# Optimization experiments

Hardware: AMD Instinct MI355X
Metric: run time of the kernel (lower is better)

The kernel has to match this reference:

```python
import jax, jax.numpy as jnp
import numpy as np

B, N, FIN, FOUT = 64, 784, 64, 64
EPS = 1e-5
NEG = -1e9  # masked-logit fill (avoids -inf NaNs on isolated nodes)


def setup_inputs() -> dict:
    key = jax.random.key(0)
    ks = jax.random.split(key, 6)
    init = lambda k, shape, fan: (jax.random.normal(k, shape, jnp.float32) / np.float32(np.sqrt(fan)))
    return {
        "node_features": jax.random.normal(ks[0], (B, N, FIN), jnp.float32),
        "adjacency_matrix": jax.random.randint(ks[1], (N, N), 0, 2, jnp.int32),
        "W_self": init(ks[2], (FOUT, FIN), FIN),
        "b_self": jnp.zeros((FOUT,), jnp.float32),
        "W_nb": init(ks[3], (FOUT, FIN), FIN),
        "b_nb": jnp.zeros((FOUT,), jnp.float32),
        "a_src": init(ks[4], (FIN,), 2 * FIN),   # attention weight half acting on x_i
        "a_dst": init(ks[5], (FIN,), 2 * FIN),   # attention weight half acting on x_j
        "b_att": jnp.zeros((), jnp.float32),
        "ln_gamma": jnp.ones((FOUT,), jnp.float32),
        "ln_beta": jnp.zeros((FOUT,), jnp.float32),
    }


def reference(node_features, adjacency_matrix, W_self, b_self, W_nb, b_nb,
              a_src, a_dst, b_att, ln_gamma, ln_beta):
    # mask[i, j] = node j is a neighbor of node i
    mask = adjacency_matrix != 0  # [N, N]

    self_feats = node_features @ W_self.T + b_self      # [B, N, Fout]
    nb_proj = node_features @ W_nb.T + b_nb              # [B, N, Fout]

    # attention(cat[x_i, x_j]) == x_i @ a_src + x_j @ a_dst + b_att
    src = node_features @ a_src                          # [B, N]
    dst = node_features @ a_dst                          # [B, N]
    logits = src[:, :, None] + dst[:, None, :] + b_att   # [B, N, N]
    logits = jnp.where(mask[None], logits, NEG)
    # softmax over neighbors j; zero out non-edges (handles isolated nodes -> 0)
    w = jax.nn.softmax(logits, axis=2) * mask[None]
    agg = jnp.einsum('bij,bjf->bif', w, nb_proj)         # [B, N, Fout]

    combined = self_feats + agg                           # dropout: eval mode (identity)
    mu = combined.mean(-1, keepdims=True)
    var = combined.var(-1, keepdims=True)
    normed = (combined - mu) * jax.lax.rsqrt(var + EPS) * ln_gamma + ln_beta
    return jax.nn.relu(normed)
```

## Files before the change

### kernel.cpp

```cpp
#include <hip/hip_runtime.h>


typedef unsigned short u16;
typedef unsigned int u32;
typedef short bf16x8 __attribute__((ext_vector_type(8)));
typedef float f32x4 __attribute__((ext_vector_type(4)));

#define NNODE 784
#define MP 832
#define BUFU 13312

__device__ __forceinline__ float b2f(u16 h) {
  union { u32 u; float f; } v; v.u = ((u32)h) << 16; return v.f;
}
__device__ __forceinline__ u16 f2b(float f) {
  union { float f; u32 u; } v; v.f = f;
  u32 r = (v.u + 0x7FFFu + ((v.u >> 16) & 1u)) >> 16;
  return (u16)r;
}
__device__ __forceinline__ void gload16(const u16* g, u16* l) {
  __builtin_amdgcn_global_load_lds((const __attribute__((address_space(1))) u32*)g,
                                   (__attribute__((address_space(3))) u32*)l, 16, 0, 0);
}

__global__ __launch_bounds__(256) void k_pre(const int* __restrict__ adj,
                                             const float* __restrict__ Ws,
                                             const float* __restrict__ Wn,
                                             const float* __restrict__ X,
                                             const float* __restrict__ adst,
                                             u16* __restrict__ A,
                                             u16* __restrict__ W2,
                                             u16* __restrict__ Bt) {
  const int bid = blockIdx.x;
  const int t = threadIdx.x;
  if (bid < 364) {
    int idx8 = bid * 256 + t;
    int i = idx8 / 104, j8 = idx8 - i * 104;
    __align__(16) u16 o[8];
    if (i < NNODE && j8 < 98) {
      const int4* ap = (const int4*)(adj + (size_t)i * NNODE + j8 * 8);
      int4 a0 = ap[0], a1 = ap[1];
      o[0] = a0.x ? 0x3F80 : 0; o[1] = a0.y ? 0x3F80 : 0;
      o[2] = a0.z ? 0x3F80 : 0; o[3] = a0.w ? 0x3F80 : 0;
      o[4] = a1.x ? 0x3F80 : 0; o[5] = a1.y ? 0x3F80 : 0;
      o[6] = a1.z ? 0x3F80 : 0; o[7] = a1.w ? 0x3F80 : 0;
    } else {
#pragma unroll
      for (int q = 0; q < 8; ++q) o[q] = 0;
    }
    *(uint4*)(A + (size_t)i * MP + j8 * 8) = *(const uint4*)o;
    return;
  }
  if (bid == 364) {
    int f = t >> 2, cq = t & 3;
#pragma unroll
    for (int q = 0; q < 4; ++q) {
      int c = cq * 4 + q;
      int cs = c ^ (f & 7);
      const float* src = (cs < 8) ? (Ws + f * 64 + cs * 8) : (Wn + f * 64 + (cs - 8) * 8);
      float4 v0 = ((const float4*)src)[0], v1 = ((const float4*)src)[1];
      __align__(16) u16 ob[8];
      ob[0] = f2b(v0.x); ob[1] = f2b(v0.y); ob[2] = f2b(v0.z); ob[3] = f2b(v0.w);
      ob[4] = f2b(v1.x); ob[5] = f2b(v1.y); ob[6] = f2b(v1.z); ob[7] = f2b(v1.w);
      *(uint4*)(W2 + f * 128 + c * 8) = *(const uint4*)ob;
    }
    return;
  }
  __shared__ float Xs[64][68];
  __shared__ float ad[64];
  __shared__ float es[64];
  int bid2 = bid - 365;
  int b = bid2 / 13, jt = bid2 - b * 13;
  int j0 = jt * 64;
  if (b == 64) {
    int row = 4160 + (t >> 2), c = (t & 3) * 16;
    uint4 z; z.x = 0; z.y = 0; z.z = 0; z.w = 0;
    uint4* p = (uint4*)(Bt + (size_t)row * MP + j0 + c);
    p[0] = z; p[1] = z;
    return;
  }
  int jr = t >> 2, cg = t & 3;
  {
    int j = j0 + jr;
    float4 z4; z4.x = 0.f; z4.y = 0.f; z4.z = 0.f; z4.w = 0.f;
    float4 v0 = z4, v1 = z4, v2 = z4, v3 = z4;
    if (j < NNODE) {
      const float4* xp = (const float4*)(X + ((size_t)b * NNODE + j) * 64 + cg * 16);
      v0 = xp[0]; v1 = xp[1]; v2 = xp[2]; v3 = xp[3];
    }
    float4* d = (float4*)&Xs[jr][cg * 16];
    d[0] = v0; d[1] = v1; d[2] = v2; d[3] = v3;
  }
  if (t < 64) ad[t] = adst[t];
  __syncthreads();
  {
    float dot = 0.f;
#pragma unroll
    for (int q = 0; q < 16; ++q) dot += Xs[jr][cg * 16 + q] * ad[cg * 16 + q];
    dot += __shfl_xor(dot, 1);
    dot += __shfl_xor(dot, 2);
    if (cg == 0) es[jr] = (j0 + jr < NNODE) ? __expf(dot) : 0.f;
  }
  __syncthreads();
  {
    int f = t >> 2, jc = (t & 3) * 16;
    __align__(16) u16 ob[16];
#pragma unroll
    for (int q = 0; q < 16; ++q) ob[q] = f2b(es[jc + q] * Xs[jc + q][f]);
    u16* op = Bt + ((size_t)b * 64 + f) * MP + j0 + jc;
    *(uint4*)op = *(const uint4*)ob;
    *(uint4*)(op + 8) = *(const uint4*)(ob + 8);
  }
  if (t < 64) Bt[(size_t)(4096 + b) * MP + j0 + t] = f2b(es[t]);
}

__global__ __launch_bounds__(512, 6) void k_gt(const u16* __restrict__ A,
                                               const u16* __restrict__ Bt,
                                               const u16* __restrict__ W2g,
                                               const float* __restrict__ X,
                                               const float* __restrict__ bs,
                                               const float* __restrict__ bn,
                                               const float* __restrict__ gam,
                                               const float* __restrict__ bet,
                                               float* __restrict__ out) {
  __shared__ __align__(16) u16 lds[2 * BUFU];
  const int t = threadIdx.x;
  const int l = t & 63, w = t >> 6;
  const int g = l >> 4, l15 = l & 15;
  const int wr = w >> 2, wc = w & 3;

  int wg = (blockIdx.x & 7) * 52 + (blockIdx.x >> 3);
  const int bp = wg / 13;
  const int it = wg - bp * 13;
  const int i0 = it * 64;
  const int nb0 = bp * 128;
  const int nd0 = 4096 + 2 * bp;

  f32x4 acc[2][2];
#pragma unroll
  for (int mi = 0; mi < 2; ++mi)
#pragma unroll
    for (int ni = 0; ni < 2; ++ni) acc[mi][ni] = (f32x4){0.f, 0.f, 0.f, 0.f};
  f32x4 accD[2];
  accD[0] = (f32x4){0.f, 0.f, 0.f, 0.f};
  accD[1] = (f32x4){0.f, 0.f, 0.f, 0.f};

#define STAGE(kt_, buf_)                                                          \
  {                                                                               \
    int k0_ = (kt_) * 64;                                                         \
    u16* dA_ = lds + (buf_) * BUFU;                                               \
    u16* dB_ = dA_ + 4096;                                                        \
    { int r_ = t >> 3, c_ = t & 7;                                                \
      gload16(A + (size_t)(i0 + r_) * MP + k0_ + ((c_ ^ (r_ & 7)) * 8),           \
              dA_ + w * 512); }                                                   \
    _Pragma("unroll")                                                             \
    for (int h_ = 0; h_ < 2; ++h_) {                                              \
      int s_ = h_ * 512 + t; int r_ = s_ >> 3, c_ = s_ & 7;                       \
      gload16(Bt + (size_t)(nb0 + r_) * MP + k0_ + ((c_ ^ (r_ & 7)) * 8),         \
              dB_ + h_ * 4096 + w * 512); }                                       \
    if (w < 2) { int r_ = t >> 3, c_ = t & 7;                                     \
      gload16(Bt + (size_t)(nd0 + r_) * MP + k0_ + ((c_ ^ (r_ & 7)) * 8),         \
              dB_ + 8192 + w * 512); }                                            \
  }

  STAGE(0, 0);

  for (int kt = 0; kt < 13; ++kt) {
    int buf = kt & 1;
    if (kt < 12) {
      STAGE(kt + 1, buf ^ 1);
      if (w < 2) asm volatile("s_waitcnt vmcnt(4)" ::: "memory");
      else       asm volatile("s_waitcnt vmcnt(3)" ::: "memory");
    } else {
      asm volatile("s_waitcnt vmcnt(0)" ::: "memory");
    }
    __builtin_amdgcn_s_barrier();
    __builtin_amdgcn_sched_barrier(0);
    const u16* As = lds + buf * BUFU;
    const u16* Bs = As + 4096;
#pragma unroll
    for (int kk = 0; kk < 2; ++kk) {
      int q = kk * 4 + g;
      bf16x8 af[2], bfr[2];
#pragma unroll
      for (int mi = 0; mi < 2; ++mi) {
        int ra = wr * 32 + mi * 16 + l15;
        af[mi] = *(const bf16x8*)(As + ra * 64 + ((q ^ (ra & 7)) * 8));
      }
#pragma unroll
      for (int ni = 0; ni < 2; ++ni) {
        int rb = wc * 32 + ni * 16 + l15;
        bfr[ni] = *(const bf16x8*)(Bs + rb * 64 + ((q ^ (rb & 7)) * 8));
      }
#pragma unroll
      for (int mi = 0; mi < 2; ++mi)
#pragma unroll
        for (int ni = 0; ni < 2; ++ni)
          acc[mi][ni] = __builtin_amdgcn_mfma_f32_16x16x32_bf16(af[mi], bfr[ni], acc[mi][ni], 0, 0, 0);
      if (wc == 2 + kk) {
        int rd = 128 + l15;
        bf16x8 bd = *(const bf16x8*)(Bs + rd * 64 + ((q ^ (rd & 7)) * 8));
        accD[0] = __builtin_amdgcn_mfma_f32_16x16x32_bf16(af[0], bd, accD[0], 0, 0, 0);
        accD[1] = __builtin_amdgcn_mfma_f32_16x16x32_bf16(af[1], bd, accD[1], 0, 0, 0);
      }
    }
    __builtin_amdgcn_sched_barrier(0);
    __builtin_amdgcn_s_barrier();
  }
#undef STAGE

  u16* AB2 = lds;
  u16* W2l = lds + 16384;
  float (*denL)[2] = (float (*)[2])((char*)lds + 49152);

  if (wc == 2 && l15 < 2) {
#pragma unroll
    for (int mi = 0; mi < 2; ++mi)
#pragma unroll
      for (int j = 0; j < 4; ++j)
        denL[wr * 32 + mi * 16 + g * 4 + j][l15] = accD[mi][j];
  }
#pragma unroll
  for (int q2 = 0; q2 < 2; ++q2) {
    int s = q2 * 512 + t;
    int r = s >> 3, c = s & 7;
    int i = i0 + (r & 63);
    int bq = bp * 2 + (r >> 6);
    float4 v0, v1;
    v0.x = v0.y = v0.z = v0.w = 0.f; v1 = v0;
    if (i < NNODE) {
      const float4* xp = (const float4*)(X + ((size_t)bq * NNODE + i) * 64 + c * 8);
      v0 = xp[0]; v1 = xp[1];
    }
    __align__(16) u16 ob[8];
    ob[0] = f2b(v0.x); ob[1] = f2b(v0.y); ob[2] = f2b(v0.z); ob[3] = f2b(v0.w);
    ob[4] = f2b(v1.x); ob[5] = f2b(v1.y); ob[6] = f2b(v1.z); ob[7] = f2b(v1.w);
    *(uint4*)(AB2 + r * 128 + ((c ^ (r & 7)) * 8)) = *(const uint4*)ob;
  }
#pragma unroll
  for (int q2 = 0; q2 < 2; ++q2)
    gload16(W2g + q2 * 4096 + w * 512 + l * 8, W2l + q2 * 4096 + w * 512);
  __syncthreads();

  if (wc == 3 && l15 < 2) {
#pragma unroll
    for (int mi = 0; mi < 2; ++mi)
#pragma unroll
      for (int j = 0; j < 4; ++j)
        denL[wr * 32 + mi * 16 + g * 4 + j][l15] += accD[mi][j];
  }
  __syncthreads();

#pragma unroll
  for (int mi = 0; mi < 2; ++mi)
#pragma unroll
    for (int ni = 0; ni < 2; ++ni) {
      int col = wc * 32 + ni * 16 + l15;
      int b2 = col >> 6, f = col & 63;
#pragma unroll
      for (int j = 0; j < 4; ++j) {
        int ri = wr * 32 + mi * 16 + g * 4 + j;
        float d = denL[ri][b2];
        float rd = d > 0.f ? 1.f / d : 0.f;
        int R = b2 * 64 + ri;
        AB2[R * 128 + (((8 + (f >> 3)) ^ (R & 7)) * 8) + (f & 7)] = f2b(acc[mi][ni][j] * rd);
      }
    }
  __syncthreads();

  const int b2w = w >> 2, mf = w & 3;
  f32x4 a2[4];
#pragma unroll
  for (int nf = 0; nf < 4; ++nf) a2[nf] = (f32x4){0.f, 0.f, 0.f, 0.f};
#pragma unroll
  for (int kk = 0; kk < 4; ++kk) {
    int q2 = kk * 4 + g;
    int ra = b2w * 64 + mf * 16 + l15;
    bf16x8 af = *(const bf16x8*)(AB2 + ra * 128 + ((q2 ^ (ra & 7)) * 8));
#pragma unroll
    for (int nf = 0; nf < 4; ++nf) {
      int rb = nf * 16 + l15;
      bf16x8 bfw = *(const bf16x8*)(W2l + rb * 128 + ((q2 ^ (rb & 7)) * 8));
      a2[nf] = __builtin_amdgcn_mfma_f32_16x16x32_bf16(af, bfw, a2[nf], 0, 0, 0);
    }
  }

  const float bs0 = bs[l15],      bn0 = bn[l15],      ga0 = gam[l15],      be0 = bet[l15];
  const float bs1 = bs[l15 + 16], bn1 = bn[l15 + 16], ga1 = gam[l15 + 16], be1 = bet[l15 + 16];
  const float bs2 = bs[l15 + 32], bn2 = bn[l15 + 32], ga2 = gam[l15 + 32], be2 = bet[l15 + 32];
  const float bs3 = bs[l15 + 48], bn3 = bn[l15 + 48], ga3 = gam[l15 + 48], be3 = bet[l15 + 48];
#pragma unroll
  for (int j = 0; j < 4; ++j) {
    int ri = mf * 16 + g * 4 + j;
    float d = denL[ri][b2w];
    float bnm = d > 0.f ? 1.f : 0.f;
    float v0 = a2[0][j] + bs0 + bnm * bn0;
    float v1 = a2[1][j] + bs1 + bnm * bn1;
    float v2 = a2[2][j] + bs2 + bnm * bn2;
    float v3 = a2[3][j] + bs3 + bnm * bn3;
    float s1 = v0 + v1 + v2 + v3;
    float s2 = v0 * v0 + v1 * v1 + v2 * v2 + v3 * v3;
    s1 += __shfl_xor(s1, 1); s2 += __shfl_xor(s2, 1);
    s1 += __shfl_xor(s1, 2); s2 += __shfl_xor(s2, 2);
    s1 += __shfl_xor(s1, 4); s2 += __shfl_xor(s2, 4);
    s1 += __shfl_xor(s1, 8); s2 += __shfl_xor(s2, 8);
    float mu = s1 * (1.f / 64.f);
    float var = fmaxf(s2 * (1.f / 64.f) - mu * mu, 0.f);
    float inv = rsqrtf(var + 1e-5f);
    int node = i0 + ri;
    if (node < NNODE) {
      float* op = out + ((size_t)(bp * 2 + b2w) * NNODE + node) * 64;
      op[l15]      = fmaxf((v0 - mu) * inv * ga0 + be0, 0.f);
      op[l15 + 16] = fmaxf((v1 - mu) * inv * ga1 + be1, 0.f);
      op[l15 + 32] = fmaxf((v2 - mu) * inv * ga2 + be2, 0.f);
      op[l15 + 48] = fmaxf((v3 - mu) * inv * ga3 + be3, 0.f);
    }
  }
}

extern "C" void kernel_launch(void* const* d_in, const int* in_sizes, int n_in,
                              void* d_out, int out_size, void* d_ws, size_t ws_size,
                              hipStream_t stream) {
  const float* X     = (const float*)d_in[0];
  const int*   adj   = (const int*)d_in[1];
  const float* Wself = (const float*)d_in[2];
  const float* bself = (const float*)d_in[3];
  const float* Wnb   = (const float*)d_in[4];
  const float* bnb   = (const float*)d_in[5];
  const float* adst  = (const float*)d_in[7];
  const float* gam   = (const float*)d_in[9];
  const float* bet   = (const float*)d_in[10];
  float* out = (float*)d_out;
  char* ws = (char*)d_ws;

  u16* Apad = (u16*)(ws);
  u16* W2g  = (u16*)(ws + 1490944);
  u16* Bt   = (u16*)(ws + 1507328);

  k_pre<<<dim3(1210), dim3(256), 0, stream>>>(adj, Wself, Wnb, X, adst, Apad, W2g, Bt);
  k_gt <<<dim3(416),  dim3(512), 0, stream>>>(Apad, Bt, W2g, X, bself, bnb, gam, bet, out);
}
```

Measured before the change: 28.61 us.

## Split K across wave halves with larger per-wave N tiles and LDS reduction

Reassigns the 8 waves so two groups each handle half of every 64-wide K slice, with each wave computing a 32x64 output tile instead of 32x32. This raises A-fragment reuse and cuts LDS fragment reads per MFMA in the main loop. Partial sums and attention denominators from the second K-group are then reduced through LDS before the normalization epilogue. The trade-off is an extra fp32 reduction pass with an added barrier and doubled accumulator registers.

```diff
diff --git a/kernel.cpp b/kernel.cpp
--- a/kernel.cpp
+++ b/kernel.cpp
@@ -127,7 +127,9 @@
   const int t = threadIdx.x;
   const int l = t & 63, w = t >> 6;
   const int g = l >> 4, l15 = l & 15;
-  const int wr = w >> 2, wc = w & 3;
+  const int kh = w >> 2;
+  const int wq = w & 3;
+  const int wr2 = wq >> 1, wc2 = wq & 1;
 
   int wg = (blockIdx.x & 7) * 52 + (blockIdx.x >> 3);
   const int bp = wg / 13;
@@ -136,11 +138,11 @@
   const int nb0 = bp * 128;
   const int nd0 = 4096 + 2 * bp;
 
-  f32x4 acc[2][2];
+  f32x4 acc[2][4];
 #pragma unroll
   for (int mi = 0; mi < 2; ++mi)
 #pragma unroll
-    for (int ni = 0; ni < 2; ++ni) acc[mi][ni] = (f32x4){0.f, 0.f, 0.f, 0.f};
+    for (int nf = 0; nf < 4; ++nf) acc[mi][nf] = (f32x4){0.f, 0.f, 0.f, 0.f};
   f32x4 accD[2];
   accD[0] = (f32x4){0.f, 0.f, 0.f, 0.f};
   accD[1] = (f32x4){0.f, 0.f, 0.f, 0.f};
@@ -178,26 +180,25 @@
     __builtin_amdgcn_sched_barrier(0);
     const u16* As = lds + buf * BUFU;
     const u16* Bs = As + 4096;
-#pragma unroll
-    for (int kk = 0; kk < 2; ++kk) {
-      int q = kk * 4 + g;
-      bf16x8 af[2], bfr[2];
+    {
+      int q = kh * 4 + g;
+      bf16x8 af[2], bfr[4];
 #pragma unroll
       for (int mi = 0; mi < 2; ++mi) {
-        int ra = wr * 32 + mi * 16 + l15;
+        int ra = wr2 * 32 + mi * 16 + l15;
         af[mi] = *(const bf16x8*)(As + ra * 64 + ((q ^ (ra & 7)) * 8));
       }
 #pragma unroll
-      for (int ni = 0; ni < 2; ++ni) {
-        int rb = wc * 32 + ni * 16 + l15;
-        bfr[ni] = *(const bf16x8*)(Bs + rb * 64 + ((q ^ (rb & 7)) * 8));
+      for (int nf = 0; nf < 4; ++nf) {
+        int rb = wc2 * 64 + nf * 16 + l15;
+        bfr[nf] = *(const bf16x8*)(Bs + rb * 64 + ((q ^ (rb & 7)) * 8));
       }
 #pragma unroll
       for (int mi = 0; mi < 2; ++mi)
 #pragma unroll
-        for (int ni = 0; ni < 2; ++ni)
-          acc[mi][ni] = __builtin_amdgcn_mfma_f32_16x16x32_bf16(af[mi], bfr[ni], acc[mi][ni], 0, 0, 0);
-      if (wc == 2 + kk) {
+        for (int nf = 0; nf < 4; ++nf)
+          acc[mi][nf] = __builtin_amdgcn_mfma_f32_16x16x32_bf16(af[mi], bfr[nf], acc[mi][nf], 0, 0, 0);
+      if (wc2 == 1) {
         int rd = 128 + l15;
         bf16x8 bd = *(const bf16x8*)(Bs + rd * 64 + ((q ^ (rd & 7)) * 8));
         accD[0] = __builtin_amdgcn_mfma_f32_16x16x32_bf16(af[0], bd, accD[0], 0, 0, 0);
@@ -209,16 +210,56 @@
   }
 #undef STAGE
 
+  float* red = (float*)lds;
   u16* AB2 = lds;
   u16* W2l = lds + 16384;
   float (*denL)[2] = (float (*)[2])((char*)lds + 49152);
 
-  if (wc == 2 && l15 < 2) {
+  if (kh == 1) {
 #pragma unroll
     for (int mi = 0; mi < 2; ++mi)
 #pragma unroll
+      for (int nf = 0; nf < 4; ++nf) {
+        int col = wc2 * 64 + nf * 16 + l15;
+#pragma unroll
+        for (int j = 0; j < 4; ++j)
+          red[(wr2 * 32 + mi * 16 + g * 4 + j) * 128 + col] = acc[mi][nf][j];
+      }
+    if (wc2 == 1 && l15 < 2) {
+#pragma unroll
+      for (int mi = 0; mi < 2; ++mi)
+#pragma unroll
+        for (int j = 0; j < 4; ++j)
+          denL[wr2 * 32 + mi * 16 + g * 4 + j][l15] = accD[mi][j];
+    }
+  }
+  __syncthreads();
+  if (kh == 0) {
+#pragma unroll
+    for (int mi = 0; mi < 2; ++mi)
+#pragma unroll
+      for (int nf = 0; nf < 4; ++nf) {
+        int col = wc2 * 64 + nf * 16 + l15;
+#pragma unroll
+        for (int j = 0; j < 4; ++j)
+          acc[mi][nf][j] += red[(wr2 * 32 + mi * 16 + g * 4 + j) * 128 + col];
+      }
+    if (wc2 == 1 && l15 < 2) {
+#pragma unroll
+      for (int mi = 0; mi < 2; ++mi)
+#pragma unroll
+        for (int j = 0; j < 4; ++j)
+          accD[mi][j] += denL[wr2 * 32 + mi * 16 + g * 4 + j][l15];
+    }
+  }
+  __syncthreads();
+
+  if (kh == 0 && wc2 == 1 && l15 < 2) {
+#pragma unroll
+    for (int mi = 0; mi < 2; ++mi)
+#pragma unroll
       for (int j = 0; j < 4; ++j)
-        denL[wr * 32 + mi * 16 + g * 4 + j][l15] = accD[mi][j];
+        denL[wr2 * 32 + mi * 16 + g * 4 + j][l15] = accD[mi][j];
   }
 #pragma unroll
   for (int q2 = 0; q2 < 2; ++q2) {
@@ -242,30 +283,23 @@
     gload16(W2g + q2 * 4096 + w * 512 + l * 8, W2l + q2 * 4096 + w * 512);
   __syncthreads();
 
-  if (wc == 3 && l15 < 2) {
+  if (kh == 0) {
 #pragma unroll
     for (int mi = 0; mi < 2; ++mi)
 #pragma unroll
-      for (int j = 0; j < 4; ++j)
-        denL[wr * 32 + mi * 16 + g * 4 + j][l15] += accD[mi][j];
-  }
-  __syncthreads();
-
-#pragma unroll
-  for (int mi = 0; mi < 2; ++mi)
-#pragma unroll
-    for (int ni = 0; ni < 2; ++ni) {
-      int col = wc * 32 + ni * 16 + l15;
-      int b2 = col >> 6, f = col & 63;
-#pragma unroll
-      for (int j = 0; j < 4; ++j) {
-        int ri = wr * 32 + mi * 16 + g * 4 + j;
-        float d = denL[ri][b2];
-        float rd = d > 0.f ? 1.f / d : 0.f;
-        int R = b2 * 64 + ri;
-        AB2[R * 128 + (((8 + (f >> 3)) ^ (R & 7)) * 8) + (f & 7)] = f2b(acc[mi][ni][j] * rd);
-      }
-    }
+      for (int nf = 0; nf < 4; ++nf) {
+        int col = wc2 * 64 + nf * 16 + l15;
+        int b2 = col >> 6, f = col & 63;
+#pragma unroll
+        for (int j = 0; j < 4; ++j) {
+          int ri = wr2 * 32 + mi * 16 + g * 4 + j;
+          float d = denL[ri][b2];
+          float rd = d > 0.f ? 1.f / d : 0.f;
+          int R = b2 * 64 + ri;
+          AB2[R * 128 + (((8 + (f >> 3)) ^ (R & 7)) * 8) + (f & 7)] = f2b(acc[mi][nf][j] * rd);
+        }
+      }
+  }
   __syncthreads();
 
   const int b2w = w >> 2, mf = w & 3;
```

After: 47.59 us. 66.4% more time.
